# Performance work log

Hardware: AMD Instinct MI355X
Metric: run time of the kernel (lower is better)

The kernel has to match this reference:

```python
import jax, jax.numpy as jnp
import numpy as np

N_NODES = 100000
N_EDGES = 1600000


def gcn_norm(row, col, num_nodes):
    # deg = bincount(row); norm_e = deg^{-1/2}[row] * deg^{-1/2}[col]
    deg = jax.ops.segment_sum(jnp.ones_like(row, dtype=jnp.float32), row,
                              num_segments=num_nodes)
    deg_inv_sqrt = 1.0 / jnp.sqrt(deg + 1e-12)
    return deg_inv_sqrt[row] * deg_inv_sqrt[col]


def graph_conv(x, row, col, norm, W):
    # H = A_norm @ (X W): gather by col, scale by edge norm, scatter-add by row
    xW = x @ W                                   # [N, out]
    msg = xW[col] * norm[:, None]                # [E, out]
    return jax.ops.segment_sum(msg, row, num_segments=x.shape[0])


def setup_inputs() -> dict:
    key = jax.random.key(0)
    k1, k2, k3, k4, k5 = jax.random.split(key, 5)
    x = jax.random.normal(k1, (N_NODES, 32), dtype=jnp.float32)
    edge_index = jax.random.randint(k2, (2, N_EDGES), 0, N_NODES, dtype=jnp.int64)
    W1 = jax.random.normal(k3, (32, 48), dtype=jnp.float32) * (1.0 / np.sqrt(32))
    W2 = jax.random.normal(k4, (48, 48), dtype=jnp.float32) * (1.0 / np.sqrt(48))
    W_out = jax.random.normal(k5, (48, 8), dtype=jnp.float32) * (1.0 / np.sqrt(48))
    return {"x": x, "edge_index": edge_index, "W1": W1, "W2": W2, "W_out": W_out}


def reference(x, edge_index, W1, W2, W_out):
    row, col = edge_index[0], edge_index[1]
    norm = gcn_norm(row, col, x.shape[0])
    h = jax.nn.relu(graph_conv(x, row, col, norm, W1))
    h = jax.nn.relu(graph_conv(h, row, col, norm, W2))
    return graph_conv(h, row, col, norm, W_out)
```

## Files before the change

kernel.cpp:

```cpp
#include <hip/hip_runtime.h>
#include <hip/hip_bf16.h>
#include <cstdint>
#include <cstddef>

static constexpr int NN = 100000;
static constexpr int NE = 1600000;
static constexpr int NB = 391;
static constexpr int GB = 250;
static constexpr int CHUNK = NE / GB;
static constexpr int MCNT = NB * GB;

typedef __attribute__((ext_vector_type(8))) short bf16x8;
typedef __attribute__((ext_vector_type(4))) float f32x4;

static __device__ __forceinline__ unsigned short f2bf(float f) {
  unsigned u = __float_as_uint(f);
  unsigned r = (u + 0x7fffu + ((u >> 16) & 1u)) >> 16;
  return (unsigned short)r;
}


__global__ __launch_bounds__(256) void k_hist(const int* __restrict__ row,
                                              int* __restrict__ counts) {
  __shared__ int hist[NB];
  for (int k = threadIdx.x; k < NB; k += 256) hist[k] = 0;
  __syncthreads();
  int g = blockIdx.x;
  int start = g * CHUNK;
  for (int gi = threadIdx.x; gi < CHUNK / 4; gi += 256) {
    int4 r4 = *reinterpret_cast<const int4*>(row + start + gi * 4);
    atomicAdd(&hist[r4.x >> 8], 1);
    atomicAdd(&hist[r4.y >> 8], 1);
    atomicAdd(&hist[r4.z >> 8], 1);
    atomicAdd(&hist[r4.w >> 8], 1);
  }
  __syncthreads();
  for (int k = threadIdx.x; k < NB; k += 256) counts[k * GB + g] = hist[k];
}


__global__ __launch_bounds__(256) void k_bsumG(const int* __restrict__ a,
                                               int* __restrict__ bsum, int M) {
  __shared__ int s[256];
  int i = blockIdx.x * 256 + threadIdx.x;
  s[threadIdx.x] = (i < M) ? a[i] : 0;
  __syncthreads();
  for (int off = 128; off > 0; off >>= 1) {
    if (threadIdx.x < off) s[threadIdx.x] += s[threadIdx.x + off];
    __syncthreads();
  }
  if (threadIdx.x == 0) bsum[blockIdx.x] = s[0];
}

__global__ __launch_bounds__(256) void k_scan_bsum(int* __restrict__ bsum, int nb) {
  __shared__ int s[256];
  __shared__ int carry;
  if (threadIdx.x == 0) carry = 0;
  __syncthreads();
  for (int base = 0; base < nb; base += 256) {
    int i = base + threadIdx.x;
    int v = (i < nb) ? bsum[i] : 0;
    s[threadIdx.x] = v;
    __syncthreads();
    for (int off = 1; off < 256; off <<= 1) {
      int t = (threadIdx.x >= off) ? s[threadIdx.x - off] : 0;
      __syncthreads();
      s[threadIdx.x] += t;
      __syncthreads();
    }
    int exc = carry + s[threadIdx.x] - v;
    if (i < nb) bsum[i] = exc;
    int tile_total = s[255];
    __syncthreads();
    if (threadIdx.x == 0) carry += tile_total;
    __syncthreads();
  }
}

__global__ __launch_bounds__(256) void k_scan_finalG(int* __restrict__ a,
                                                     const int* __restrict__ bsum,
                                                     int M) {
  __shared__ int s[256];
  int i = blockIdx.x * 256 + threadIdx.x;
  int v = (i < M) ? a[i] : 0;
  s[threadIdx.x] = v;
  __syncthreads();
  for (int off = 1; off < 256; off <<= 1) {
    int t = (threadIdx.x >= off) ? s[threadIdx.x - off] : 0;
    __syncthreads();
    s[threadIdx.x] += t;
    __syncthreads();
  }
  if (i < M) a[i] = bsum[blockIdx.x] + s[threadIdx.x] - v;
}


__global__ __launch_bounds__(256) void k_bucket(const int* __restrict__ row,
                                                const int* __restrict__ col,
                                                const int* __restrict__ counts,
                                                unsigned int* __restrict__ packed) {
  __shared__ int cur[NB];
  int g = blockIdx.x;
  for (int k = threadIdx.x; k < NB; k += 256) cur[k] = counts[k * GB + g];
  __syncthreads();
  int start = g * CHUNK;
  for (int gi = threadIdx.x; gi < CHUNK / 4; gi += 256) {
    int4 r4 = *reinterpret_cast<const int4*>(row + start + gi * 4);
    int4 c4 = *reinterpret_cast<const int4*>(col + start + gi * 4);
    int p0 = atomicAdd(&cur[r4.x >> 8], 1);
    int p1 = atomicAdd(&cur[r4.y >> 8], 1);
    int p2 = atomicAdd(&cur[r4.z >> 8], 1);
    int p3 = atomicAdd(&cur[r4.w >> 8], 1);
    packed[p0] = ((unsigned)(r4.x & 255) << 17) | (unsigned)c4.x;
    packed[p1] = ((unsigned)(r4.y & 255) << 17) | (unsigned)c4.y;
    packed[p2] = ((unsigned)(r4.z & 255) << 17) | (unsigned)c4.z;
    packed[p3] = ((unsigned)(r4.w & 255) << 17) | (unsigned)c4.w;
  }
}


__global__ __launch_bounds__(256) void k_csr(const unsigned int* __restrict__ packed,
                                             const int* __restrict__ counts,
                                             int* __restrict__ rowptr,
                                             float* __restrict__ dis,
                                             int* __restrict__ csr_col,
                                             const float* __restrict__ x,
                                             unsigned short* __restrict__ xb,
                                             int N, int E) {
  __shared__ int rh[256];
  __shared__ int sc[256];
  __shared__ int cur[256];
  __shared__ float ldis[256];
  int b = blockIdx.x;
  int start = counts[b * GB];
  int end = (b + 1 < NB) ? counts[(b + 1) * GB] : E;

  rh[threadIdx.x] = 0;
  __syncthreads();
  for (int i = start + threadIdx.x; i < end; i += 256)
    atomicAdd(&rh[packed[i] >> 17], 1);
  __syncthreads();

  int v = rh[threadIdx.x];
  sc[threadIdx.x] = v;
  __syncthreads();
  for (int off = 1; off < 256; off <<= 1) {
    int t = (threadIdx.x >= off) ? sc[threadIdx.x - off] : 0;
    __syncthreads();
    sc[threadIdx.x] += t;
    __syncthreads();
  }
  int exc = sc[threadIdx.x] - v;

  float dv = 1.0f / sqrtf((float)v + 1e-12f);
  ldis[threadIdx.x] = dv;
  int gr = (b << 8) + threadIdx.x;
  if (gr < N) {
    rowptr[gr] = start + exc;
    dis[gr] = dv;
  }
  if (b == NB - 1 && threadIdx.x == 0) rowptr[N] = E;

  cur[threadIdx.x] = exc;
  __syncthreads();
  for (int i = start + threadIdx.x; i < end; i += 256) {
    unsigned p = packed[i];
    int lr = p >> 17;
    int c = (int)(p & 0x1FFFFu);
    int pos = atomicAdd(&cur[lr], 1);
    csr_col[start + pos] = c;
  }

  int rows = min(256, N - (b << 8));
  if (rows > 0) {
    const float4* xs = reinterpret_cast<const float4*>(x + ((size_t)b << 8) * 32);
    ushort4* xd = reinterpret_cast<ushort4*>(xb + ((size_t)b << 8) * 32);
    for (int i = threadIdx.x; i < rows * 8; i += 256) {
      float ds = ldis[i >> 3];
      float4 vv = xs[i];
      xd[i] = make_ushort4(f2bf(vv.x * ds), f2bf(vv.y * ds),
                           f2bf(vv.z * ds), f2bf(vv.w * ds));
    }
  }
}


template <int SQ>
static __device__ __forceinline__ void acc_bf(float* acc, const uint4* u) {
#pragma unroll
  for (int q = 0; q < SQ; ++q) {
    acc[8 * q + 0] += __uint_as_float(u[q].x << 16);
    acc[8 * q + 1] += __uint_as_float(u[q].x & 0xffff0000u);
    acc[8 * q + 2] += __uint_as_float(u[q].y << 16);
    acc[8 * q + 3] += __uint_as_float(u[q].y & 0xffff0000u);
    acc[8 * q + 4] += __uint_as_float(u[q].z << 16);
    acc[8 * q + 5] += __uint_as_float(u[q].z & 0xffff0000u);
    acc[8 * q + 6] += __uint_as_float(u[q].w << 16);
    acc[8 * q + 7] += __uint_as_float(u[q].w & 0xffff0000u);
  }
}


__global__ __launch_bounds__(256) void k_gather_bf1(const uint4* __restrict__ src,
                                                    const int* __restrict__ rowptr,
                                                    const int* __restrict__ csr_col,
                                                    const float* __restrict__ dis,
                                                    unsigned short* __restrict__ dst,
                                                    int N) {
  int t = blockIdx.x * 256 + threadIdx.x;
  int r = t >> 2, g = t & 3;
  if (r >= N) return;
  int j = rowptr[r], end = rowptr[r + 1];

  float acc[8];
#pragma unroll
  for (int q = 0; q < 8; ++q) acc[q] = 0.f;

  for (; j + 4 <= end; j += 4) {
    int c0 = csr_col[j], c1 = csr_col[j + 1], c2 = csr_col[j + 2], c3 = csr_col[j + 3];
    uint4 u0 = src[(size_t)c0 * 4 + g];
    uint4 u1 = src[(size_t)c1 * 4 + g];
    uint4 u2 = src[(size_t)c2 * 4 + g];
    uint4 u3 = src[(size_t)c3 * 4 + g];
    acc_bf<1>(acc, &u0);
    acc_bf<1>(acc, &u1);
    acc_bf<1>(acc, &u2);
    acc_bf<1>(acc, &u3);
  }
  for (; j < end; ++j) {
    uint4 u0 = src[(size_t)csr_col[j] * 4 + g];
    acc_bf<1>(acc, &u0);
  }

  float ds = dis[r];
  uint4 pk;
  unsigned* pw = reinterpret_cast<unsigned*>(&pk);
#pragma unroll
  for (int i = 0; i < 4; ++i)
    pw[i] = (unsigned)f2bf(ds * acc[2 * i]) |
            ((unsigned)f2bf(ds * acc[2 * i + 1]) << 16);
  *reinterpret_cast<uint4*>(dst + (size_t)r * 32 + g * 8) = pk;
}


__global__ __launch_bounds__(256) void k_gemm12_mfma(
    const unsigned short* __restrict__ g1b,
    const float* __restrict__ W1,
    const float* __restrict__ W2,
    const float* __restrict__ dis,
    unsigned short* __restrict__ s2,
    int N) {
  __shared__ __align__(16) unsigned short hl[4][16][72];

  int w = threadIdx.x >> 6;
  int l = threadIdx.x & 63;
  int c = l & 15;
  int g = l >> 4;
  int rb = blockIdx.x * 64 + w * 16;
  int r = rb + c;
  int rc = min(r, N - 1);

  bf16x8 w1f[3];
#pragma unroll
  for (int t = 0; t < 3; ++t) {
#pragma unroll
    for (int i = 0; i < 8; ++i)
      w1f[t][i] = (short)f2bf(W1[(g * 8 + i) * 48 + 16 * t + c]);
  }
  bf16x8 w2f[3][2];
#pragma unroll
  for (int t = 0; t < 3; ++t) {
#pragma unroll
    for (int s = 0; s < 2; ++s) {
#pragma unroll
      for (int i = 0; i < 8; ++i) {
        int k = s * 32 + g * 8 + i;
        w2f[t][s][i] = (k < 48) ? (short)f2bf(W2[k * 48 + 16 * t + c]) : (short)0;
      }
    }
  }

  bf16x8 bfr = *reinterpret_cast<const bf16x8*>(g1b + (size_t)rc * 32 + g * 8);
  f32x4 a1[3];
#pragma unroll
  for (int t = 0; t < 3; ++t) {
    a1[t] = f32x4{0.f, 0.f, 0.f, 0.f};
    a1[t] = __builtin_amdgcn_mfma_f32_16x16x32_bf16(w1f[t], bfr, a1[t], 0, 0, 0);
  }

#pragma unroll
  for (int t = 0; t < 3; ++t) {
    int f = 16 * t + 4 * g;
    unsigned p0 = (unsigned)f2bf(fmaxf(a1[t][0], 0.f)) |
                  ((unsigned)f2bf(fmaxf(a1[t][1], 0.f)) << 16);
    unsigned p1 = (unsigned)f2bf(fmaxf(a1[t][2], 0.f)) |
                  ((unsigned)f2bf(fmaxf(a1[t][3], 0.f)) << 16);
    *reinterpret_cast<unsigned*>(&hl[w][c][f]) = p0;
    *reinterpret_cast<unsigned*>(&hl[w][c][f + 2]) = p1;
  }
  *reinterpret_cast<unsigned*>(&hl[w][c][48 + 4 * g]) = 0u;
  *reinterpret_cast<unsigned*>(&hl[w][c][48 + 4 * g + 2]) = 0u;

  f32x4 a2[3];
#pragma unroll
  for (int t = 0; t < 3; ++t) a2[t] = f32x4{0.f, 0.f, 0.f, 0.f};
#pragma unroll
  for (int s = 0; s < 2; ++s) {
    bf16x8 hb = *reinterpret_cast<const bf16x8*>(&hl[w][c][s * 32 + 8 * g]);
#pragma unroll
    for (int t = 0; t < 3; ++t)
      a2[t] = __builtin_amdgcn_mfma_f32_16x16x32_bf16(w2f[t][s], hb, a2[t], 0, 0, 0);
  }

  float ds = dis[rc];
#pragma unroll
  for (int t = 0; t < 3; ++t) {
    int f = 16 * t + 4 * g;
    unsigned p0 = (unsigned)f2bf(ds * a2[t][0]) |
                  ((unsigned)f2bf(ds * a2[t][1]) << 16);
    unsigned p1 = (unsigned)f2bf(ds * a2[t][2]) |
                  ((unsigned)f2bf(ds * a2[t][3]) << 16);
    *reinterpret_cast<unsigned*>(&hl[w][c][f]) = p0;
    *reinterpret_cast<unsigned*>(&hl[w][c][f + 2]) = p1;
  }
#pragma unroll
  for (int h2 = 0; h2 < 2; ++h2) {
    int q = l + 64 * h2;
    int rowq = q >> 3, off = q & 7;
    int rr = rb + rowq;
    if (rr < N) {
      uint4 v = *reinterpret_cast<const uint4*>(&hl[w][rowq][off * 8]);
      *reinterpret_cast<uint4*>(s2 + (size_t)rr * 64 + off * 8) = v;
    }
  }
}


__global__ __launch_bounds__(256) void k_gather_fc(const uint4* __restrict__ src,
                                                   const int* __restrict__ rowptr,
                                                   const int* __restrict__ csr_col,
                                                   const float* __restrict__ dis,
                                                   const float* __restrict__ Wo,
                                                   float* __restrict__ s3, int N) {
  __shared__ float Wol[64 * 8];
  for (int i = threadIdx.x; i < 512; i += 256) Wol[i] = (i < 384) ? Wo[i] : 0.f;
  __syncthreads();

  int t = blockIdx.x * 256 + threadIdx.x;
  int r = t >> 3, g = t & 7;
  if (r >= N) return;
  int j = rowptr[r], end = rowptr[r + 1];

  float acc[8];
#pragma unroll
  for (int q = 0; q < 8; ++q) acc[q] = 0.f;

  for (; j + 4 <= end; j += 4) {
    int c0 = csr_col[j], c1 = csr_col[j + 1], c2 = csr_col[j + 2], c3 = csr_col[j + 3];
    uint4 u0 = src[(size_t)c0 * 8 + g];
    uint4 u1 = src[(size_t)c1 * 8 + g];
    uint4 u2 = src[(size_t)c2 * 8 + g];
    uint4 u3 = src[(size_t)c3 * 8 + g];
    acc_bf<1>(acc, &u0);
    acc_bf<1>(acc, &u1);
    acc_bf<1>(acc, &u2);
    acc_bf<1>(acc, &u3);
  }
  for (; j < end; ++j) {
    uint4 u0 = src[(size_t)csr_col[j] * 8 + g];
    acc_bf<1>(acc, &u0);
  }

  float ds = dis[r];
  float v[8];
#pragma unroll
  for (int q = 0; q < 8; ++q) v[q] = fmaxf(ds * acc[q], 0.f);

  float p[8];
#pragma unroll
  for (int n = 0; n < 8; ++n) p[n] = 0.f;
  const int base = g * 8;
#pragma unroll
  for (int q = 0; q < 8; ++q) {
    float4 w0 = *reinterpret_cast<const float4*>(&Wol[(base + q) * 8]);
    float4 w1 = *reinterpret_cast<const float4*>(&Wol[(base + q) * 8 + 4]);
    p[0] = fmaf(v[q], w0.x, p[0]);
    p[1] = fmaf(v[q], w0.y, p[1]);
    p[2] = fmaf(v[q], w0.z, p[2]);
    p[3] = fmaf(v[q], w0.w, p[3]);
    p[4] = fmaf(v[q], w1.x, p[4]);
    p[5] = fmaf(v[q], w1.y, p[5]);
    p[6] = fmaf(v[q], w1.z, p[6]);
    p[7] = fmaf(v[q], w1.w, p[7]);
  }
#pragma unroll
  for (int m = 1; m < 8; m <<= 1) {
#pragma unroll
    for (int n = 0; n < 8; ++n) p[n] += __shfl_xor(p[n], m, 64);
  }
  if (g < 2) {
    float4 w = make_float4(ds * p[4 * g + 0], ds * p[4 * g + 1],
                           ds * p[4 * g + 2], ds * p[4 * g + 3]);
    *reinterpret_cast<float4*>(s3 + (size_t)r * 8 + 4 * g) = w;
  }
}


template <int LPR, int FQ>
__global__ __launch_bounds__(256) void k_gather(const float* __restrict__ src,
                                                const int* __restrict__ rowptr,
                                                const int* __restrict__ csr_col,
                                                const float* __restrict__ dis,
                                                float* __restrict__ dst, int N) {
  constexpr int F = LPR * FQ * 4;
  int t = blockIdx.x * 256 + threadIdx.x;
  int r = t / LPR, g = t % LPR;
  if (r >= N) return;
  int j = rowptr[r], end = rowptr[r + 1];

  float acc[FQ * 4];
#pragma unroll
  for (int q = 0; q < FQ * 4; ++q) acc[q] = 0.f;

  for (; j + 2 <= end; j += 2) {
    int c0 = csr_col[j], c1 = csr_col[j + 1];
    const float4* sp0 =
        reinterpret_cast<const float4*>(src + (size_t)c0 * F + g * (FQ * 4));
    const float4* sp1 =
        reinterpret_cast<const float4*>(src + (size_t)c1 * F + g * (FQ * 4));
    float4 v0[FQ], v1[FQ];
#pragma unroll
    for (int q = 0; q < FQ; ++q) v0[q] = sp0[q];
#pragma unroll
    for (int q = 0; q < FQ; ++q) v1[q] = sp1[q];
#pragma unroll
    for (int q = 0; q < FQ; ++q) {
      acc[4 * q + 0] += v0[q].x + v1[q].x;
      acc[4 * q + 1] += v0[q].y + v1[q].y;
      acc[4 * q + 2] += v0[q].z + v1[q].z;
      acc[4 * q + 3] += v0[q].w + v1[q].w;
    }
  }
  if (j < end) {
    int c0 = csr_col[j];
    const float4* sp0 =
        reinterpret_cast<const float4*>(src + (size_t)c0 * F + g * (FQ * 4));
#pragma unroll
    for (int q = 0; q < FQ; ++q) {
      float4 v = sp0[q];
      acc[4 * q + 0] += v.x;
      acc[4 * q + 1] += v.y;
      acc[4 * q + 2] += v.z;
      acc[4 * q + 3] += v.w;
    }
  }

  float ds = dis[r];
  float4* dp = reinterpret_cast<float4*>(dst + (size_t)r * F + g * (FQ * 4));
#pragma unroll
  for (int q = 0; q < FQ; ++q)
    dp[q] = make_float4(ds * acc[4 * q + 0], ds * acc[4 * q + 1],
                        ds * acc[4 * q + 2], ds * acc[4 * q + 3]);
}


extern "C" void kernel_launch(void* const* d_in, const int* in_sizes, int n_in,
                              void* d_out, int out_size, void* d_ws, size_t ws_size,
                              hipStream_t stream) {
  const float* x  = (const float*)d_in[0];
  const int*   ei = (const int*)d_in[1];
  const float* W1 = (const float*)d_in[2];
  const float* W2 = (const float*)d_in[3];
  const float* Wo = (const float*)d_in[4];
  float* out = (float*)d_out;

  const int N = NN, E = NE;
  const int* row = ei;
  const int* col = ei + E;
  const int scanG = (MCNT + 255) / 256;

  int*   counts  = (int*)d_ws;
  int*   bsum    = counts + 97752;
  int*   rowptr  = bsum + 384;
  float* dis     = (float*)(rowptr + 100008);
  int*   csr_col = (int*)(dis + 100000);
  float* A1      = (float*)(csr_col + NE);
  float* A2      = A1 + 3200000;
  float* s3      = A2 + 4000000;
  unsigned int*   packed = (unsigned int*)A1;
  unsigned short* s2     = (unsigned short*)A1;
  unsigned short* g1b    = (unsigned short*)A2;
  unsigned short* xb     = (unsigned short*)(A2 + 3200000);

  k_hist<<<GB, 256, 0, stream>>>(row, counts);
  k_bsumG<<<scanG, 256, 0, stream>>>(counts, bsum, MCNT);
  k_scan_bsum<<<1, 256, 0, stream>>>(bsum, scanG);
  k_scan_finalG<<<scanG, 256, 0, stream>>>(counts, bsum, MCNT);
  k_bucket<<<GB, 256, 0, stream>>>(row, col, counts, packed);
  k_csr<<<NB, 256, 0, stream>>>(packed, counts, rowptr, dis, csr_col, x, xb, N, E);

  k_gather_bf1<<<(N * 4 + 255) / 256, 256, 0, stream>>>(
      (const uint4*)xb, rowptr, csr_col, dis, g1b, N);

  k_gemm12_mfma<<<(N + 63) / 64, 256, 0, stream>>>(g1b, W1, W2, dis, s2, N);

  k_gather_fc<<<(N * 8 + 255) / 256, 256, 0, stream>>>(
      (const uint4*)s2, rowptr, csr_col, dis, Wo, s3, N);

  k_gather<2, 1><<<(N * 2 + 255) / 256, 256, 0, stream>>>(s3, rowptr, csr_col,
                                                          dis, out, N);
}
```

Measured before the change: 141.5 us.

## Restructure count scan into per-bucket scans and sort CSR columns by quarter

The three-kernel global scan over the bucket-by-block count matrix becomes two kernels: a per-bucket exclusive scan that also writes bucket totals, and a single-block scan that turns those totals into bucket bases. This removes one launch and one pass over the counts. Separately, the CSR build now splits each row's edges into four sub-buckets by column range, so column indices within a row are roughly grouped by range. That should improve locality in the later gathers over the node features, at the cost of larger shared histograms and a few compares per edge.

```diff
diff --git a/kernel.cpp b/kernel.cpp
--- a/kernel.cpp
+++ b/kernel.cpp
@@ -8,7 +8,6 @@
 static constexpr int NB = 391;
 static constexpr int GB = 250;
 static constexpr int CHUNK = NE / GB;
-static constexpr int MCNT = NB * GB;
 
 typedef __attribute__((ext_vector_type(8))) short bf16x8;
 typedef __attribute__((ext_vector_type(4))) float f32x4;
@@ -17,6 +16,10 @@
   unsigned u = __float_as_uint(f);
   unsigned r = (u + 0x7fffu + ((u >> 16) & 1u)) >> 16;
   return (unsigned short)r;
+}
+
+static __device__ __forceinline__ int quarter(int c) {
+  return (c >= 50000) ? ((c >= 75000) ? 3 : 2) : ((c >= 25000) ? 1 : 0);
 }
 
 
@@ -39,27 +42,34 @@
 }
 
 
-__global__ __launch_bounds__(256) void k_bsumG(const int* __restrict__ a,
-                                               int* __restrict__ bsum, int M) {
+__global__ __launch_bounds__(256) void k_scanA(int* __restrict__ counts,
+                                               int* __restrict__ totals) {
   __shared__ int s[256];
-  int i = blockIdx.x * 256 + threadIdx.x;
-  s[threadIdx.x] = (i < M) ? a[i] : 0;
-  __syncthreads();
-  for (int off = 128; off > 0; off >>= 1) {
-    if (threadIdx.x < off) s[threadIdx.x] += s[threadIdx.x + off];
-    __syncthreads();
-  }
-  if (threadIdx.x == 0) bsum[blockIdx.x] = s[0];
-}
-
-__global__ __launch_bounds__(256) void k_scan_bsum(int* __restrict__ bsum, int nb) {
+  int k = blockIdx.x;
+  int i = threadIdx.x;
+  int v = (i < GB) ? counts[k * GB + i] : 0;
+  s[i] = v;
+  __syncthreads();
+  for (int off = 1; off < 256; off <<= 1) {
+    int t = (i >= off) ? s[i - off] : 0;
+    __syncthreads();
+    s[i] += t;
+    __syncthreads();
+  }
+  if (i < GB) counts[k * GB + i] = s[i] - v;
+  if (i == 255) totals[k] = s[255];
+}
+
+
+__global__ __launch_bounds__(256) void k_scanB(const int* __restrict__ totals,
+                                               int* __restrict__ bases, int nb) {
   __shared__ int s[256];
   __shared__ int carry;
   if (threadIdx.x == 0) carry = 0;
   __syncthreads();
   for (int base = 0; base < nb; base += 256) {
     int i = base + threadIdx.x;
-    int v = (i < nb) ? bsum[i] : 0;
+    int v = (i < nb) ? totals[i] : 0;
     s[threadIdx.x] = v;
     __syncthreads();
     for (int off = 1; off < 256; off <<= 1) {
@@ -69,39 +79,25 @@
       __syncthreads();
     }
     int exc = carry + s[threadIdx.x] - v;
-    if (i < nb) bsum[i] = exc;
+    if (i < nb) bases[i] = exc;
     int tile_total = s[255];
     __syncthreads();
     if (threadIdx.x == 0) carry += tile_total;
     __syncthreads();
   }
-}
-
-__global__ __launch_bounds__(256) void k_scan_finalG(int* __restrict__ a,
-                                                     const int* __restrict__ bsum,
-                                                     int M) {
-  __shared__ int s[256];
-  int i = blockIdx.x * 256 + threadIdx.x;
-  int v = (i < M) ? a[i] : 0;
-  s[threadIdx.x] = v;
-  __syncthreads();
-  for (int off = 1; off < 256; off <<= 1) {
-    int t = (threadIdx.x >= off) ? s[threadIdx.x - off] : 0;
-    __syncthreads();
-    s[threadIdx.x] += t;
-    __syncthreads();
-  }
-  if (i < M) a[i] = bsum[blockIdx.x] + s[threadIdx.x] - v;
+  if (threadIdx.x == 0) bases[nb] = carry;
 }
 
 
 __global__ __launch_bounds__(256) void k_bucket(const int* __restrict__ row,
                                                 const int* __restrict__ col,
                                                 const int* __restrict__ counts,
+                                                const int* __restrict__ bases,
                                                 unsigned int* __restrict__ packed) {
   __shared__ int cur[NB];
   int g = blockIdx.x;
-  for (int k = threadIdx.x; k < NB; k += 256) cur[k] = counts[k * GB + g];
+  for (int k = threadIdx.x; k < NB; k += 256)
+    cur[k] = bases[k] + counts[k * GB + g];
   __syncthreads();
   int start = g * CHUNK;
   for (int gi = threadIdx.x; gi < CHUNK / 4; gi += 256) {
@@ -120,29 +116,37 @@
 
 
 __global__ __launch_bounds__(256) void k_csr(const unsigned int* __restrict__ packed,
-                                             const int* __restrict__ counts,
+                                             const int* __restrict__ bases,
                                              int* __restrict__ rowptr,
                                              float* __restrict__ dis,
                                              int* __restrict__ csr_col,
                                              const float* __restrict__ x,
                                              unsigned short* __restrict__ xb,
                                              int N, int E) {
-  __shared__ int rh[256];
+  __shared__ int rq[256 * 4];
   __shared__ int sc[256];
-  __shared__ int cur[256];
+  __shared__ int cur[256 * 4];
   __shared__ float ldis[256];
   int b = blockIdx.x;
-  int start = counts[b * GB];
-  int end = (b + 1 < NB) ? counts[(b + 1) * GB] : E;
-
-  rh[threadIdx.x] = 0;
-  __syncthreads();
-  for (int i = start + threadIdx.x; i < end; i += 256)
-    atomicAdd(&rh[packed[i] >> 17], 1);
-  __syncthreads();
-
-  int v = rh[threadIdx.x];
-  sc[threadIdx.x] = v;
+  int start = bases[b];
+  int end = bases[b + 1];
+
+  for (int k = threadIdx.x; k < 1024; k += 256) rq[k] = 0;
+  __syncthreads();
+  for (int i = start + threadIdx.x; i < end; i += 256) {
+    unsigned p = packed[i];
+    int lr = p >> 17;
+    int c = (int)(p & 0x1FFFFu);
+    atomicAdd(&rq[lr * 4 + quarter(c)], 1);
+  }
+  __syncthreads();
+
+  int n0 = rq[threadIdx.x * 4 + 0];
+  int n1 = rq[threadIdx.x * 4 + 1];
+  int n2 = rq[threadIdx.x * 4 + 2];
+  int n3 = rq[threadIdx.x * 4 + 3];
+  int deg = n0 + n1 + n2 + n3;
+  sc[threadIdx.x] = deg;
   __syncthreads();
   for (int off = 1; off < 256; off <<= 1) {
     int t = (threadIdx.x >= off) ? sc[threadIdx.x - off] : 0;
@@ -150,9 +154,14 @@
     sc[threadIdx.x] += t;
     __syncthreads();
   }
-  int exc = sc[threadIdx.x] - v;
-
-  float dv = 1.0f / sqrtf((float)v + 1e-12f);
+  int exc = sc[threadIdx.x] - deg;
+
+  cur[threadIdx.x * 4 + 0] = exc;
+  cur[threadIdx.x * 4 + 1] = exc + n0;
+  cur[threadIdx.x * 4 + 2] = exc + n0 + n1;
+  cur[threadIdx.x * 4 + 3] = exc + n0 + n1 + n2;
+
+  float dv = 1.0f / sqrtf((float)deg + 1e-12f);
   ldis[threadIdx.x] = dv;
   int gr = (b << 8) + threadIdx.x;
   if (gr < N) {
@@ -160,14 +169,13 @@
     dis[gr] = dv;
   }
   if (b == NB - 1 && threadIdx.x == 0) rowptr[N] = E;
-
-  cur[threadIdx.x] = exc;
-  __syncthreads();
+  __syncthreads();
+
   for (int i = start + threadIdx.x; i < end; i += 256) {
     unsigned p = packed[i];
     int lr = p >> 17;
     int c = (int)(p & 0x1FFFFu);
-    int pos = atomicAdd(&cur[lr], 1);
+    int pos = atomicAdd(&cur[lr * 4 + quarter(c)], 1);
     csr_col[start + pos] = c;
   }
 
@@ -477,11 +485,11 @@
   const int N = NN, E = NE;
   const int* row = ei;
   const int* col = ei + E;
-  const int scanG = (MCNT + 255) / 256;
 
   int*   counts  = (int*)d_ws;
-  int*   bsum    = counts + 97752;
-  int*   rowptr  = bsum + 384;
+  int*   totals  = counts + 97752;
+  int*   bases   = totals + 392;
+  int*   rowptr  = bases + 400;
   float* dis     = (float*)(rowptr + 100008);
   int*   csr_col = (int*)(dis + 100000);
   float* A1      = (float*)(csr_col + NE);
@@ -493,11 +501,10 @@
   unsigned short* xb     = (unsigned short*)(A2 + 3200000);
 
   k_hist<<<GB, 256, 0, stream>>>(row, counts);
-  k_bsumG<<<scanG, 256, 0, stream>>>(counts, bsum, MCNT);
-  k_scan_bsum<<<1, 256, 0, stream>>>(bsum, scanG);
-  k_scan_finalG<<<scanG, 256, 0, stream>>>(counts, bsum, MCNT);
-  k_bucket<<<GB, 256, 0, stream>>>(row, col, counts, packed);
-  k_csr<<<NB, 256, 0, stream>>>(packed, counts, rowptr, dis, csr_col, x, xb, N, E);
+  k_scanA<<<NB, 256, 0, stream>>>(counts, totals);
+  k_scanB<<<1, 256, 0, stream>>>(totals, bases, NB);
+  k_bucket<<<GB, 256, 0, stream>>>(row, col, counts, bases, packed);
+  k_csr<<<NB, 256, 0, stream>>>(packed, bases, rowptr, dis, csr_col, x, xb, N, E);
 
   k_gather_bf1<<<(N * 4 + 255) / 256, 256, 0, stream>>>(
       (const uint4*)xb, rowptr, csr_col, dis, g1b, N);
```

New measurement: 154.4 us. 1.09x slower.
